# Kernel tuning notes

Hardware: AMD Instinct MI355X
Metric: run time of the kernel (lower is better)

Reference implementation:

```python
import jax, jax.numpy as jnp
import numpy as np

F = 256          # number of features (input_size)
H1, H2, H3 = 128, 64, 32
OUT = 1          # output_size


def setup_inputs() -> dict:
    key = jax.random.key(0)
    ks = jax.random.split(key, 10)
    B = 8192
    # Kaiming-uniform-ish small init; exact init doesn't matter for a math reference.
    def w(k, shape, fan_in):
        lim = 1.0 / np.sqrt(fan_in)
        return jax.random.uniform(k, shape, jnp.float32, -lim, lim)
    return {
        "x": jax.random.normal(ks[0], (B, F), dtype=jnp.float32),
        "W1": w(ks[1], (F, H1), 1),          # Linear(1 -> H1) per feature
        "b1": w(ks[2], (F, H1), 1),
        "W2": w(ks[3], (F, H1, H2), H1),
        "b2": w(ks[4], (F, H2), H1),
        "W3": w(ks[5], (F, H2, H3), H2),
        "b3": w(ks[6], (F, H3), H2),
        "W4": w(ks[7], (F, H3, OUT), H3),
        "b4": w(ks[8], (F, OUT), H3),
        "bias": jnp.zeros((OUT,), dtype=jnp.float32),
    }


def reference(x, W1, b1, W2, b2, W3, b3, W4, b4, bias):
    # Fused form of the per-feature FeatureNN loop (eval mode: dropout = identity).
    # Layer 1: scalar input per feature -> H1
    h = jax.nn.relu(x[:, :, None] * W1[None, :, :] + b1[None, :, :])   # [B,F,H1]
    h = jax.nn.relu(jnp.einsum('bfh,fhk->bfk', h, W2) + b2[None])      # [B,F,H2]
    h = jax.nn.relu(jnp.einsum('bfh,fhk->bfk', h, W3) + b3[None])      # [B,F,H3]
    f_out = jnp.einsum('bfh,fhk->bfk', h, W4) + b4[None]               # [B,F,OUT]
    # torch.cat(dim=1).sum(dim=1, keepdim=True): sum over features and output cols
    out = jnp.sum(f_out, axis=(1, 2), keepdims=False)[:, None] + bias[None, :]
    return out  # [B, OUT] with OUT==1
```

## Files before the change

### kernel.cpp

```cpp
#include <hip/hip_runtime.h>
#include <math.h>


#define NF   256
#define NH1  128
#define NH2  64
#define NH3  32
#define NB   8192

#define NRANK 129
#define ROW4  17
#define ROWH  136

typedef float    f32x16 __attribute__((ext_vector_type(16)));
typedef unsigned u32x4  __attribute__((ext_vector_type(4)));
typedef _Float16 h16x2  __attribute__((ext_vector_type(2)));
typedef _Float16 h16x8  __attribute__((ext_vector_type(8)));

__device__ __forceinline__ unsigned pkh2(unsigned sw, unsigned sb, h16x2 xh) {
    h16x2 r = __builtin_elementwise_fma(xh, __builtin_bit_cast(h16x2, sw),
                                            __builtin_bit_cast(h16x2, sb));
    h16x2 hz = {(_Float16)0.f, (_Float16)0.f};
    return __builtin_bit_cast(unsigned, __builtin_elementwise_max(r, hz));
}

__global__ __launch_bounds__(1024) void transpose_x(
    const float* __restrict__ x, const float* __restrict__ bias,
    float* __restrict__ out, float* __restrict__ xt)
{
    __shared__ float xtile[64][65];
    const int t = (int)threadIdx.x;
    const int T = blockIdx.x;
    const int bt = T >> 2, ft = T & 3;

    if (T < 8) out[T * 1024 + t] = bias[0];

    #pragma unroll
    for (int it = 0; it < 4; ++it) {
        int idx = t + it * 1024;
        int rr = idx >> 6, cc = idx & 63;
        xtile[rr][cc] = x[(size_t)(bt * 64 + rr) * NF + ft * 64 + cc];
    }
    __syncthreads();
    #pragma unroll
    for (int it = 0; it < 4; ++it) {
        int idx = t + it * 1024;
        int cc = idx >> 6, rr = idx & 63;
        xt[(size_t)(ft * 64 + cc) * NB + bt * 64 + rr] = xtile[rr][cc];
    }
}

__global__ __launch_bounds__(1024) void nam_fused(
    const float* __restrict__ W1, const float* __restrict__ b1,
    const float* __restrict__ W2, const float* __restrict__ b2,
    const float* __restrict__ W3, const float* __restrict__ b3,
    const float* __restrict__ W4, const float* __restrict__ b4,
    const float* __restrict__ xt,
    float* __restrict__ out)
{
    __shared__ u32x4 SP4[NRANK * ROW4];
    __shared__ float rkey[NH1];
    __shared__ float skey[NH1];
    __shared__ int   sidx[NH1];
    __shared__ float w1s[NH1], b1s[NH1];
    __shared__ float Pbw[16][NH2], Pbb[16][NH2], Pdw[16][NH2], Pdb[16][NH2];
    __shared__ float lv8[8], lv4[16], lv2[32], lv1[64];

    const int f = blockIdx.x;
    const int t = (int)threadIdx.x;
    _Float16* SPh = (_Float16*)SP4;

    const float* __restrict__ gw2 = W2 + (size_t)f * NH1 * NH2;
    if (t < NH1) {
        float w  = W1[f * NH1 + t];
        float bb = b1[f * NH1 + t];
        w1s[t] = w; b1s[t] = bb;
        rkey[t] = (w != 0.0f) ? (-bb / w) : INFINITY;
    }
    __syncthreads();

    if (t < NH1) {
        const float my = rkey[t];
        int rk = 0;
        #pragma unroll 16
        for (int i = 0; i < NH1; ++i) {
            float ki = rkey[i];
            rk += (ki < my || (ki == my && i < t)) ? 1 : 0;
        }
        skey[rk] = my; sidx[rk] = t;
    }
    __syncthreads();

    if (t < 8)            lv8[t]      = skey[t * 16 + 7];
    else if (t < 24)      lv4[t - 8]  = skey[(t - 8) * 8 + 3];
    else if (t < 56)      lv2[t - 24] = skey[(t - 24) * 4 + 1];
    else if (t < 120)     lv1[t - 56] = skey[(t - 56) * 2];

    {
        const int k = t & 63, c = t >> 6;
        float bw = 0.0f, bbp = 0.0f, dw = 0.0f, db = 0.0f;
        #pragma unroll
        for (int i = 0; i < 8; ++i) {
            int j = c * 8 + i;
            float w = w1s[j], bv = b1s[j], w2v = gw2[j * NH2 + k];
            if (w < 0.0f) { bw = fmaf(w, w2v, bw); bbp = fmaf(bv, w2v, bbp); }
            else if (w == 0.0f && bv > 0.0f) { bbp = fmaf(bv, w2v, bbp); }
            int jj = sidx[c * 8 + i];
            float ww = w1s[jj], bv2 = b1s[jj], w2x = gw2[jj * NH2 + k];
            float s = (ww > 0.0f) ? 1.0f : ((ww < 0.0f) ? -1.0f : 0.0f);
            dw = fmaf(s * ww,  w2x, dw);
            db = fmaf(s * bv2, w2x, db);
        }
        Pbw[c][k] = bw; Pbb[c][k] = bbp; Pdw[c][k] = dw; Pdb[c][k] = db;
    }
    __syncthreads();
    {
        const int k = t & 63, c = t >> 6;
        float accw = 0.0f;
        float accb = b2[f * NH2 + k];
        #pragma unroll
        for (int c2 = 0; c2 < 16; ++c2) { accw += Pbw[c2][k]; accb += Pbb[c2][k]; }
        for (int c2 = 0; c2 < c; ++c2) { accw += Pdw[c2][k]; accb += Pdb[c2][k]; }
        if (c == 0) {
            SPh[k]      = (_Float16)accw;
            SPh[64 + k] = (_Float16)accb;
        }
        #pragma unroll
        for (int i = 0; i < 8; ++i) {
            int r = c * 8 + i;
            int j = sidx[r];
            float w = w1s[j], bv = b1s[j], w2v = gw2[j * NH2 + k];
            float s = (w > 0.0f) ? 1.0f : ((w < 0.0f) ? -1.0f : 0.0f);
            accw = fmaf(s * w,  w2v, accw);
            accb = fmaf(s * bv, w2v, accb);
            SPh[(r + 1) * ROWH + k]      = (_Float16)accw;
            SPh[(r + 1) * ROWH + 64 + k] = (_Float16)accb;
        }
    }
    __syncthreads();

    const int lane = t & 63, wv = t >> 6;
    const int n = lane & 31, q2 = lane >> 5;

    const float* __restrict__ w3g = W3 + f * NH2 * NH3;
    h16x8 A0, A1, A2, A3;
    #pragma unroll
    for (int j = 0; j < 8; ++j) {
        int kk = q2 * 8 + j;
        A0[j] = (_Float16)w3g[kk * NH3 + n];
        A1[j] = (_Float16)w3g[(kk + 16) * NH3 + n];
        A2[j] = (_Float16)w3g[(kk + 32) * NH3 + n];
        A3[j] = (_Float16)w3g[(kk + 48) * NH3 + n];
    }
    f32x16 bacc;
    float w4r[16];
    #pragma unroll
    for (int reg = 0; reg < 16; ++reg) {
        int row = (reg & 3) + 8 * (reg >> 2) + 4 * q2;
        bacc[reg] = b3[f * NH3 + row];
        w4r[reg]  = W4[f * NH3 + row];
    }
    const float b4f = b4[f];
    const float* __restrict__ xrow = xt + (size_t)f * NB;
    const float t63 = skey[63], t31 = skey[31], t95 = skey[95];
    const float t15 = skey[15], t47 = skey[47], t79 = skey[79], t111 = skey[111];

    auto rankof = [&](float q) -> int {
        int rr = (t63 < q) ? 64 : 0;
        {
            float l1 = (rr & 64) ? t95 : t31;
            if (l1 < q) rr += 32;
            float m0 = (rr & 64) ? t79  : t15;
            float m1 = (rr & 64) ? t111 : t47;
            float l2 = (rr & 32) ? m1 : m0;
            if (l2 < q) rr += 16;
        }
        if (lv8[rr >> 4] < q) rr += 8;
        if (lv4[rr >> 3] < q) rr += 4;
        if (lv2[rr >> 2] < q) rr += 2;
        if (lv1[rr >> 1] < q) rr += 1;
        return rr;
    };

    auto bat = [&](int round) -> int {
        return (((round + f) & 15) * 16 + wv) * 32 + n;
    };
    float xv = xrow[bat(0)];
    int r = rankof(xv);

    #pragma unroll 1
    for (int round = 0; round < 16; ++round) {
        const int base = (((round + f) & 15) * 16 + wv) * 32;
        const float xnext = xrow[bat((round + 1) & 15)];

        const int ro = r * ROW4;
        u32x4 SW0 = SP4[ro + q2],      SW1 = SP4[ro + 2 + q2];
        u32x4 SW2 = SP4[ro + 4 + q2],  SW3 = SP4[ro + 6 + q2];
        u32x4 SB0 = SP4[ro + 8 + q2],  SB1 = SP4[ro + 10 + q2];
        u32x4 SB2 = SP4[ro + 12 + q2], SB3 = SP4[ro + 14 + q2];

        const h16x2 xh = {(_Float16)xv, (_Float16)xv};
        u32x4 d0, d1, d2, d3;
        d0.x = pkh2(SW0.x, SB0.x, xh); d0.y = pkh2(SW0.y, SB0.y, xh);
        d0.z = pkh2(SW0.z, SB0.z, xh); d0.w = pkh2(SW0.w, SB0.w, xh);
        d1.x = pkh2(SW1.x, SB1.x, xh); d1.y = pkh2(SW1.y, SB1.y, xh);
        d1.z = pkh2(SW1.z, SB1.z, xh); d1.w = pkh2(SW1.w, SB1.w, xh);
        d2.x = pkh2(SW2.x, SB2.x, xh); d2.y = pkh2(SW2.y, SB2.y, xh);
        d2.z = pkh2(SW2.z, SB2.z, xh); d2.w = pkh2(SW2.w, SB2.w, xh);
        d3.x = pkh2(SW3.x, SB3.x, xh); d3.y = pkh2(SW3.y, SB3.y, xh);
        d3.z = pkh2(SW3.z, SB3.z, xh); d3.w = pkh2(SW3.w, SB3.w, xh);
        h16x8 B0 = __builtin_bit_cast(h16x8, d0);
        h16x8 B1 = __builtin_bit_cast(h16x8, d1);
        h16x8 B2 = __builtin_bit_cast(h16x8, d2);
        h16x8 B3 = __builtin_bit_cast(h16x8, d3);

        f32x16 acc = __builtin_amdgcn_mfma_f32_32x32x16_f16(A0, B0, bacc, 0, 0, 0);
        acc = __builtin_amdgcn_mfma_f32_32x32x16_f16(A1, B1, acc, 0, 0, 0);
        acc = __builtin_amdgcn_mfma_f32_32x32x16_f16(A2, B2, acc, 0, 0, 0);
        acc = __builtin_amdgcn_mfma_f32_32x32x16_f16(A3, B3, acc, 0, 0, 0);

        const int rnext = rankof(xnext);

        float p = 0.0f;
        #pragma unroll
        for (int reg = 0; reg < 16; ++reg)
            p = fmaf(fmaxf(acc[reg], 0.0f), w4r[reg], p);
        float pa = p, pb = p;
        asm volatile("v_permlane32_swap_b32 %0, %1" : "+v"(pa), "+v"(pb));
        if (lane < 32) atomicAdd(&out[base + lane], p + pb + b4f);

        xv = xnext; r = rnext;
    }
}

extern "C" void kernel_launch(void* const* d_in, const int* in_sizes, int n_in,
                              void* d_out, int out_size, void* d_ws, size_t ws_size,
                              hipStream_t stream) {
    const float* x    = (const float*)d_in[0];
    const float* W1   = (const float*)d_in[1];
    const float* b1   = (const float*)d_in[2];
    const float* W2   = (const float*)d_in[3];
    const float* b2   = (const float*)d_in[4];
    const float* W3   = (const float*)d_in[5];
    const float* b3   = (const float*)d_in[6];
    const float* W4   = (const float*)d_in[7];
    const float* b4   = (const float*)d_in[8];
    const float* bias = (const float*)d_in[9];
    float* out   = (float*)d_out;
    float* xtw   = (float*)d_ws;

    transpose_x<<<512, 1024, 0, stream>>>(x, bias, out, xtw);
    nam_fused<<<NF, 1024, 0, stream>>>(W1, b1, W2, b2, W3, b3, W4, b4,
                                       xtw, out);
}
```

Before: 111.8 us.

## Counting-sort batch elements by rank per feature to group similar LDS rows

Each feature block now computes the piecewise-linear segment rank of every batch element up front. It builds an LDS histogram with a prefix sum and writes a rank-sorted permutation, packed as index plus rank, to workspace. The main MFMA loop walks the batch in sorted order, so lanes in a wave read the same or adjacent SP4 rows, which is meant to cut LDS bank conflicts and remove the per-round rank search. The trade-off is an extra global perm write and read, gathered x loads, scattered atomics into out instead of contiguous ones, and an extra sync and serial prefix-sum phase.

New measurement: 193.2 us. +72.8%, slower.

```diff
diff --git a/kernel.cpp b/kernel.cpp
--- a/kernel.cpp
+++ b/kernel.cpp
@@ -55,7 +55,7 @@
     const float* __restrict__ W2, const float* __restrict__ b2,
     const float* __restrict__ W3, const float* __restrict__ b3,
     const float* __restrict__ W4, const float* __restrict__ b4,
-    const float* __restrict__ xt,
+    const float* __restrict__ xt, unsigned* __restrict__ perm,
     float* __restrict__ out)
 {
     __shared__ u32x4 SP4[NRANK * ROW4];
@@ -65,6 +65,7 @@
     __shared__ float w1s[NH1], b1s[NH1];
     __shared__ float Pbw[16][NH2], Pbb[16][NH2], Pdw[16][NH2], Pdb[16][NH2];
     __shared__ float lv8[8], lv4[16], lv2[32], lv1[64];
+    __shared__ unsigned hist[132];
 
     const int f = blockIdx.x;
     const int t = (int)threadIdx.x;
@@ -77,6 +78,7 @@
         w1s[t] = w; b1s[t] = bb;
         rkey[t] = (w != 0.0f) ? (-bb / w) : INFINITY;
     }
+    if (t >= 1024 - 132) hist[t - (1024 - 132)] = 0;
     __syncthreads();
 
     if (t < NH1) {
@@ -139,32 +141,10 @@
     }
     __syncthreads();
 
-    const int lane = t & 63, wv = t >> 6;
-    const int n = lane & 31, q2 = lane >> 5;
-
-    const float* __restrict__ w3g = W3 + f * NH2 * NH3;
-    h16x8 A0, A1, A2, A3;
-    #pragma unroll
-    for (int j = 0; j < 8; ++j) {
-        int kk = q2 * 8 + j;
-        A0[j] = (_Float16)w3g[kk * NH3 + n];
-        A1[j] = (_Float16)w3g[(kk + 16) * NH3 + n];
-        A2[j] = (_Float16)w3g[(kk + 32) * NH3 + n];
-        A3[j] = (_Float16)w3g[(kk + 48) * NH3 + n];
-    }
-    f32x16 bacc;
-    float w4r[16];
-    #pragma unroll
-    for (int reg = 0; reg < 16; ++reg) {
-        int row = (reg & 3) + 8 * (reg >> 2) + 4 * q2;
-        bacc[reg] = b3[f * NH3 + row];
-        w4r[reg]  = W4[f * NH3 + row];
-    }
-    const float b4f = b4[f];
     const float* __restrict__ xrow = xt + (size_t)f * NB;
+    unsigned* __restrict__ permf = perm + (size_t)f * NB;
     const float t63 = skey[63], t31 = skey[31], t95 = skey[95];
     const float t15 = skey[15], t47 = skey[47], t79 = skey[79], t111 = skey[111];
-
     auto rankof = [&](float q) -> int {
         int rr = (t63 < q) ? 64 : 0;
         {
@@ -182,16 +162,58 @@
         return rr;
     };
 
-    auto bat = [&](int round) -> int {
-        return (((round + f) & 15) * 16 + wv) * 32 + n;
-    };
-    float xv = xrow[bat(0)];
-    int r = rankof(xv);
+    int myr[8];
+    #pragma unroll
+    for (int i = 0; i < 8; ++i) {
+        const int e = i * 1024 + t;
+        myr[i] = rankof(xrow[e]);
+        atomicAdd(&hist[myr[i]], 1u);
+    }
+    __syncthreads();
+    if (t == 0) {
+        unsigned run = 0;
+        for (int b = 0; b < NRANK; ++b) { unsigned c = hist[b]; hist[b] = run; run += c; }
+    }
+    __syncthreads();
+    #pragma unroll
+    for (int i = 0; i < 8; ++i) {
+        const int e = i * 1024 + t;
+        unsigned pos = atomicAdd(&hist[myr[i]], 1u);
+        permf[pos] = (unsigned)e | ((unsigned)myr[i] << 16);
+    }
+    __syncthreads();
+
+    const int lane = t & 63, wv = t >> 6;
+    const int n = lane & 31, q2 = lane >> 5;
+
+    const float* __restrict__ w3g = W3 + f * NH2 * NH3;
+    h16x8 A0, A1, A2, A3;
+    #pragma unroll
+    for (int j = 0; j < 8; ++j) {
+        int kk = q2 * 8 + j;
+        A0[j] = (_Float16)w3g[kk * NH3 + n];
+        A1[j] = (_Float16)w3g[(kk + 16) * NH3 + n];
+        A2[j] = (_Float16)w3g[(kk + 32) * NH3 + n];
+        A3[j] = (_Float16)w3g[(kk + 48) * NH3 + n];
+    }
+    f32x16 bacc;
+    float w4r[16];
+    #pragma unroll
+    for (int reg = 0; reg < 16; ++reg) {
+        int row = (reg & 3) + 8 * (reg >> 2) + 4 * q2;
+        bacc[reg] = b3[f * NH3 + row];
+        w4r[reg]  = W4[f * NH3 + row];
+    }
+    const float b4f = b4[f];
+
+    unsigned pr = permf[wv * 512 + n];
+    float   xv = xrow[pr & 0xFFFF];
 
     #pragma unroll 1
     for (int round = 0; round < 16; ++round) {
-        const int base = (((round + f) & 15) * 16 + wv) * 32;
-        const float xnext = xrow[bat((round + 1) & 15)];
+        const unsigned prn = permf[wv * 512 + ((round + 1) & 15) * 32 + n];
+
+        const int r = (int)(pr >> 16);
 
         const int ro = r * ROW4;
         u32x4 SW0 = SP4[ro + q2],      SW1 = SP4[ro + 2 + q2];
@@ -219,7 +241,7 @@
         acc = __builtin_amdgcn_mfma_f32_32x32x16_f16(A2, B2, acc, 0, 0, 0);
         acc = __builtin_amdgcn_mfma_f32_32x32x16_f16(A3, B3, acc, 0, 0, 0);
 
-        const int rnext = rankof(xnext);
+        const float xvn = xrow[prn & 0xFFFF];
 
         float p = 0.0f;
         #pragma unroll
@@ -227,9 +249,9 @@
             p = fmaf(fmaxf(acc[reg], 0.0f), w4r[reg], p);
         float pa = p, pb = p;
         asm volatile("v_permlane32_swap_b32 %0, %1" : "+v"(pa), "+v"(pb));
-        if (lane < 32) atomicAdd(&out[base + lane], p + pb + b4f);
-
-        xv = xnext; r = rnext;
+        if (lane < 32) atomicAdd(&out[pr & 0xFFFF], p + pb + b4f);
+
+        pr = prn; xv = xvn;
     }
 }
 
@@ -248,8 +270,9 @@
     const float* bias = (const float*)d_in[9];
     float* out   = (float*)d_out;
     float* xtw   = (float*)d_ws;
+    unsigned* permw = (unsigned*)d_ws + (size_t)NF * NB;
 
     transpose_x<<<512, 1024, 0, stream>>>(x, bias, out, xtw);
     nam_fused<<<NF, 1024, 0, stream>>>(W1, b1, W2, b2, W3, b3, W4, b4,
-                                       xtw, out);
-}
+                                       xtw, permw, out);
+}
```
